# Kernel tuning notes

Measured on AMD Instinct MI355X. Metric: run time of the kernel, lower is better.

## Reference

```python
import jax, jax.numpy as jnp
import numpy as np

NEG_SLOPE = 0.2  # PyG GATConv default negative_slope


def gat_conv(x, src, dst, W, att_src, att_dst, bias, heads):
    """PyG-style GATConv (concat=True). src/dst already include self-loops.
    x: [N, Fin]; W: [Fin, heads*Fout]; att_*: [heads, Fout]; bias: [heads*Fout].
    """
    N = x.shape[0]
    Fout = att_src.shape[-1]
    h = (x @ W).reshape(N, heads, Fout)              # [N, H, C]
    a_s = jnp.einsum('nhc,hc->nh', h, att_src)        # [N, H]
    a_d = jnp.einsum('nhc,hc->nh', h, att_dst)        # [N, H]
    e = jax.nn.leaky_relu(a_s[src] + a_d[dst], NEG_SLOPE)   # [E, H]
    # segment softmax over destination nodes
    m = jax.lax.stop_gradient(jax.ops.segment_max(e, dst, num_segments=N))  # [N, H]
    ex = jnp.exp(e - m[dst])
    denom = jax.ops.segment_sum(ex, dst, num_segments=N)     # [N, H]
    alpha = ex / (denom[dst] + 1e-16)                          # [E, H]
    msg = h[src] * alpha[:, :, None]                           # [E, H, C]
    out = jax.ops.segment_sum(msg, dst, num_segments=N)       # [N, H, C]
    return out.reshape(N, heads * Fout) + bias


def setup_inputs() -> dict:
    key = jax.random.key(0)
    ks = jax.random.split(key, 16)
    NU, NS, D, H, CTX, B, E = 100000, 100000, 64, 2, 3, 512, 1600000
    inp = {
        'user_idx': jax.random.randint(ks[0], (B,), 0, NU),
        'context_idx': jax.random.randint(ks[1], (B, CTX), 0, NS),
        'edge_index': jax.random.randint(ks[2], (2, E), 0, NS),
        'user_emb': jax.random.normal(ks[3], (NU, D), jnp.float32),
        'service_emb': jax.random.normal(ks[4], (NS, D), jnp.float32),
        'W1': jax.random.normal(ks[5], (D, H * D), jnp.float32) / np.sqrt(D),
        'att_src1': jax.random.normal(ks[6], (H, D), jnp.float32) / np.sqrt(D),
        'att_dst1': jax.random.normal(ks[7], (H, D), jnp.float32) / np.sqrt(D),
        'b1': jnp.zeros((H * D,), jnp.float32),
        'W2': jax.random.normal(ks[8], (H * D, D), jnp.float32) / np.sqrt(H * D),
        'att_src2': jax.random.normal(ks[9], (1, D), jnp.float32) / np.sqrt(D),
        'att_dst2': jax.random.normal(ks[10], (1, D), jnp.float32) / np.sqrt(D),
        'b2': jnp.zeros((D,), jnp.float32),
        'fc_w': jax.random.normal(ks[11], (D * (CTX + 1), NS), jnp.float32) / np.sqrt(D * (CTX + 1)),
        'fc_b': jnp.zeros((NS,), jnp.float32),
    }
    return inp


def reference(user_idx, context_idx, edge_index, user_emb, service_emb,
              W1, att_src1, att_dst1, b1, W2, att_src2, att_dst2, b2, fc_w, fc_b):
    N = service_emb.shape[0]
    loops = jnp.arange(N)
    src = jnp.concatenate([edge_index[0], loops])  # add self loops (PyG default)
    dst = jnp.concatenate([edge_index[1], loops])
    user_vec = user_emb[user_idx]                                  # [B, D]
    g = gat_conv(service_emb, src, dst, W1, att_src1, att_dst1, b1, heads=2)
    g = jax.nn.elu(g)
    g = gat_conv(g, src, dst, W2, att_src2, att_dst2, b2, heads=1)  # [N, D]
    ctx = g[context_idx]                                            # [B, CTX, D]
    ctx = ctx.reshape(ctx.shape[0], -1)
    x = jnp.concatenate([user_vec, ctx], axis=1)                    # [B, D*(CTX+1)]
    return x @ fc_w + fc_b                                           # [B, num_services]
```

## Files before the change

kernel.cpp:

```cpp
#include <hip/hip_runtime.h>
#include <hip/hip_bf16.h>
#include <math.h>

#define NEG_SLOPE 0.2f

#define NPB 512
#define NPB_SH 9
#define SRC_BITS 18
#define LCAP 16384
#define BCAP 16384

typedef __attribute__((ext_vector_type(8))) short short8;
typedef __attribute__((ext_vector_type(4))) float f32x4;

__device__ __forceinline__ float leaky(float x) { return x > 0.f ? x : NEG_SLOPE * x; }

__device__ __forceinline__ unsigned short f2bf(float f) {
  unsigned u = __float_as_uint(f);
  unsigned r = (u + 0x7FFFu + ((u >> 16) & 1u)) >> 16;
  return (unsigned short)r;
}

#define LGKM_BARRIER()                                   \
  do {                                                   \
    asm volatile("s_waitcnt lgkmcnt(0)" ::: "memory");   \
    __builtin_amdgcn_s_barrier();                        \
  } while (0)

__global__ void k_h1(const float* __restrict__ x, const float* __restrict__ W1,
                     const float* __restrict__ att_src, const float* __restrict__ att_dst,
                     unsigned short* __restrict__ h1, float* __restrict__ a_s,
                     float* __restrict__ a_d, int N) {
  __shared__ __align__(16) float W1s[64 * 128];
  __shared__ __align__(16) float xs[32][64];
  const int tid = threadIdx.x;
  for (int i = tid; i < 64 * 128; i += 256) W1s[i] = W1[i];
  const int node0 = blockIdx.x * 32;
  for (int i = tid; i < 512; i += 256) {
    const int nn = node0 + (i >> 4);
    if (nn < N) ((float4*)xs)[i] = *(const float4*)(x + (size_t)nn * 64 + (i & 15) * 4);
  }
  const int ln  = tid >> 7;
  const int col = tid & 127;
  const int head = col >> 6;
  const int c = col & 63;
  const float as_w = att_src[head * 64 + c];
  const float ad_w = att_dst[head * 64 + c];
  __syncthreads();
  float wreg[64];
#pragma unroll
  for (int cc = 0; cc < 64; ++cc) wreg[cc] = W1s[cc * 128 + col];

  for (int it = 0; it < 16; ++it) {
    const int slot = it * 2 + ln;
    const int n = node0 + slot;
    if (n >= N) continue;
    float acc = 0.f;
#pragma unroll
    for (int q = 0; q < 16; ++q) {
      const float4 xv = *(const float4*)&xs[slot][q * 4];
      acc = fmaf(xv.x, wreg[q * 4 + 0], acc);
      acc = fmaf(xv.y, wreg[q * 4 + 1], acc);
      acc = fmaf(xv.z, wreg[q * 4 + 2], acc);
      acc = fmaf(xv.w, wreg[q * 4 + 3], acc);
    }
    h1[(size_t)n * 128 + col] = f2bf(acc);
    float vs = acc * as_w;
    float vd = acc * ad_w;
#pragma unroll
    for (int off = 32; off > 0; off >>= 1) {
      vs += __shfl_down(vs, off, 64);
      vd += __shfl_down(vd, off, 64);
    }
    if (c == 0) { a_s[n * 2 + head] = vs; a_d[n * 2 + head] = vd; }
  }
}

__global__ void k_init(int* __restrict__ cursor, int NB, int* __restrict__ flagC,
                       int* __restrict__ flag1, int* __restrict__ cnt, int N) {
  const int i = blockIdx.x * 256 + threadIdx.x;
  if (i < NB) cursor[i] = i * BCAP;
  if (i < N) { flagC[i] = 0; flag1[i] = 0; }
  if (i < 2) cnt[i] = 0;
}

__global__ void k_markC(const int* __restrict__ ctx, int nctx, int* __restrict__ flagC,
                        int* __restrict__ flag1) {
  const int i = blockIdx.x * 256 + threadIdx.x;
  if (i >= nctx) return;
  const int n = ctx[i];
  flagC[n] = 1;
  flag1[n] = 1;
}

__global__ void k_markS1e(const int* __restrict__ src, const int* __restrict__ dst,
                          int E, int Etot, const int* __restrict__ flagC,
                          int* __restrict__ flag1) {
  const int e = blockIdx.x * 256 + threadIdx.x;
  if (e >= Etot) return;
  int s, d;
  if (e < E) { s = src[e]; d = dst[e]; } else { s = d = e - E; }
  if (flagC[d]) flag1[s] = 1;
}

__global__ void k_compact(const int* __restrict__ flagC, const int* __restrict__ flag1,
                          int* __restrict__ listC, int* __restrict__ list1,
                          int* __restrict__ cnt, int N) {
  __shared__ int lc, l1, bc, b1;
  const int i = blockIdx.x * 256 + threadIdx.x;
  if (threadIdx.x == 0) { lc = 0; l1 = 0; }
  __syncthreads();
  int pc = -1, p1 = -1;
  if (i < N) {
    if (flagC[i]) pc = atomicAdd(&lc, 1);
    if (flag1[i]) p1 = atomicAdd(&l1, 1);
  }
  __syncthreads();
  if (threadIdx.x == 0) {
    bc = lc ? atomicAdd(&cnt[0], lc) : 0;
    b1 = l1 ? atomicAdd(&cnt[1], l1) : 0;
  }
  __syncthreads();
  if (pc >= 0) listC[bc + pc] = i;
  if (p1 >= 0) list1[b1 + p1] = i;
}

__global__ __launch_bounds__(1024) void k_bscatter(const int* __restrict__ src,
                                                   const int* __restrict__ dst, int E, int Etot,
                                                   int epb, const int* __restrict__ flag1,
                                                   int* __restrict__ cursor,
                                                   unsigned* __restrict__ rec, int NB) {
  __shared__ int hist[256];
  __shared__ int cur[256];
  const int tid = threadIdx.x;
  if (tid < 256) hist[tid] = 0;
  __syncthreads();
  const int e0 = blockIdx.x * epb;
  const int e1 = min(e0 + epb, Etot);
  for (int e = e0 + tid; e < e1; e += 1024) {
    const int d = (e < E) ? dst[e] : (e - E);
    if (flag1[d]) atomicAdd(&hist[d >> NPB_SH], 1);
  }
  __syncthreads();
  if (tid < NB) {
    const int c = hist[tid];
    cur[tid] = c ? atomicAdd(&cursor[tid], c) : 0;
  }
  __syncthreads();
  for (int e = e0 + tid; e < e1; e += 1024) {
    int sv, d;
    if (e < E) { sv = src[e]; d = dst[e]; } else { sv = d = e - E; }
    if (!flag1[d]) continue;
    const int b = d >> NPB_SH;
    const int p = atomicAdd(&cur[b], 1);
    rec[p] = (unsigned)sv | ((unsigned)(d & (NPB - 1)) << SRC_BITS);
  }
}

__global__ __launch_bounds__(1024) void k_bcsr(const unsigned* __restrict__ rec,
                                               const int* __restrict__ cursor,
                                               int* __restrict__ rowptr, int* __restrict__ adj,
                                               int N, int NB) {
  __shared__ int ldeg[NPB];
  __shared__ int s[NPB];
  __shared__ int ladj[LCAP];
  __shared__ int o0s, cnts;
  const int b = blockIdx.x;
  const int tid = threadIdx.x;

  if (tid < 256) s[tid] = (tid < NB) ? (cursor[tid] - tid * BCAP) : 0;
  __syncthreads();
  for (int off = 1; off < 256; off <<= 1) {
    int t = 0;
    if (tid < 256 && tid >= off) t = s[tid - off];
    __syncthreads();
    if (tid < 256) s[tid] += t;
    __syncthreads();
  }
  if (tid == 0) {
    const int cb = cursor[b] - b * BCAP;
    o0s = s[b] - cb;
    cnts = cb;
    if (b == 0) rowptr[N] = s[NB - 1];
  }
  __syncthreads();
  const int o0 = o0s;
  const int cnt = cnts;
  const int r0 = b * BCAP;

  if (tid < NPB) ldeg[tid] = 0;
  __syncthreads();
  for (int i = tid; i < cnt; i += 1024)
    atomicAdd(&ldeg[rec[r0 + i] >> SRC_BITS], 1);
  __syncthreads();
  int v = 0;
  if (tid < NPB) { v = ldeg[tid]; s[tid] = v; }
  __syncthreads();
  for (int off = 1; off < NPB; off <<= 1) {
    int t = 0;
    if (tid < NPB && tid >= off) t = s[tid - off];
    __syncthreads();
    if (tid < NPB) s[tid] += t;
    __syncthreads();
  }
  if (tid < NPB) {
    const int excl = s[tid] - v;
    const int node = b * NPB + tid;
    if (node < N) rowptr[node] = o0 + excl;
    ldeg[tid] = excl;
  }
  __syncthreads();
  if (cnt <= LCAP) {
    for (int i = tid; i < cnt; i += 1024) {
      const unsigned r = rec[r0 + i];
      const int p = atomicAdd(&ldeg[r >> SRC_BITS], 1);
      ladj[p] = (int)(r & ((1u << SRC_BITS) - 1));
    }
    __syncthreads();
    for (int i = tid; i < cnt; i += 1024) adj[o0 + i] = ladj[i];
  } else {
    for (int i = tid; i < cnt; i += 1024) {
      const unsigned r = rec[r0 + i];
      const int p = atomicAdd(&ldeg[r >> SRC_BITS], 1);
      adj[o0 + p] = (int)(r & ((1u << SRC_BITS) - 1));
    }
  }
}

__global__ void k_gat1(const unsigned short* __restrict__ h1, const float* __restrict__ as1,
                       const float* __restrict__ ad1, const int* __restrict__ rowptr,
                       const int* __restrict__ adj, const float* __restrict__ b1,
                       float* __restrict__ g, const int* __restrict__ list1,
                       const int* __restrict__ cnt) {
  const int w = threadIdx.x >> 6;
  const int l = threadIdx.x & 63;
  const int idx = blockIdx.x * 4 + w;
  if (idx >= cnt[1]) return;
  const int n = list1[idx];
  const int half = l >> 5;
  const int q = l & 31;
  const int head = q >> 4;
  const float adh = ad1[n * 2 + head];
  float a0 = 0.f, a1 = 0.f, a2 = 0.f, a3 = 0.f, dsum = 0.f;
  const int kb = rowptr[n], ke = rowptr[n + 1];
  const int kend = ke - 1;
  for (int k = kb + half; k < ke; k += 8) {
    const int e1 = k + 2, e2 = k + 4, e3 = k + 6;
    const int s0 = adj[k];
    const int s1 = adj[min(e1, kend)];
    const int s2 = adj[min(e2, kend)];
    const int s3 = adj[min(e3, kend)];
    const float x0 = as1[s0 * 2 + head] + adh;
    const float x1 = as1[s1 * 2 + head] + adh;
    const float x2 = as1[s2 * 2 + head] + adh;
    const float x3 = as1[s3 * 2 + head] + adh;
    const uint2 u0 = *(const uint2*)(h1 + (size_t)s0 * 128 + 4 * q);
    const uint2 u1 = *(const uint2*)(h1 + (size_t)s1 * 128 + 4 * q);
    const uint2 u2 = *(const uint2*)(h1 + (size_t)s2 * 128 + 4 * q);
    const uint2 u3 = *(const uint2*)(h1 + (size_t)s3 * 128 + 4 * q);
    const float w0 = __expf(leaky(x0));
    const float w1 = (e1 < ke) ? __expf(leaky(x1)) : 0.f;
    const float w2 = (e2 < ke) ? __expf(leaky(x2)) : 0.f;
    const float w3 = (e3 < ke) ? __expf(leaky(x3)) : 0.f;
    dsum += (w0 + w1) + (w2 + w3);
    a0 = fmaf(w0, __uint_as_float(u0.x << 16), a0);
    a1 = fmaf(w0, __uint_as_float(u0.x & 0xFFFF0000u), a1);
    a2 = fmaf(w0, __uint_as_float(u0.y << 16), a2);
    a3 = fmaf(w0, __uint_as_float(u0.y & 0xFFFF0000u), a3);
    a0 = fmaf(w1, __uint_as_float(u1.x << 16), a0);
    a1 = fmaf(w1, __uint_as_float(u1.x & 0xFFFF0000u), a1);
    a2 = fmaf(w1, __uint_as_float(u1.y << 16), a2);
    a3 = fmaf(w1, __uint_as_float(u1.y & 0xFFFF0000u), a3);
    a0 = fmaf(w2, __uint_as_float(u2.x << 16), a0);
    a1 = fmaf(w2, __uint_as_float(u2.x & 0xFFFF0000u), a1);
    a2 = fmaf(w2, __uint_as_float(u2.y << 16), a2);
    a3 = fmaf(w2, __uint_as_float(u2.y & 0xFFFF0000u), a3);
    a0 = fmaf(w3, __uint_as_float(u3.x << 16), a0);
    a1 = fmaf(w3, __uint_as_float(u3.x & 0xFFFF0000u), a1);
    a2 = fmaf(w3, __uint_as_float(u3.y << 16), a2);
    a3 = fmaf(w3, __uint_as_float(u3.y & 0xFFFF0000u), a3);
  }
  a0 += __shfl_xor(a0, 32, 64);
  a1 += __shfl_xor(a1, 32, 64);
  a2 += __shfl_xor(a2, 32, 64);
  a3 += __shfl_xor(a3, 32, 64);
  dsum += __shfl_xor(dsum, 32, 64);
  if (half == 0) {
    const float inv = 1.f / (dsum + 1e-16f);
    const float4 bv = *(const float4*)(b1 + 4 * q);
    float g0 = fmaf(a0, inv, bv.x);
    float g1 = fmaf(a1, inv, bv.y);
    float g2v = fmaf(a2, inv, bv.z);
    float g3 = fmaf(a3, inv, bv.w);
    g0 = g0 > 0.f ? g0 : expm1f(g0);
    g1 = g1 > 0.f ? g1 : expm1f(g1);
    g2v = g2v > 0.f ? g2v : expm1f(g2v);
    g3 = g3 > 0.f ? g3 : expm1f(g3);
    *(float4*)(g + (size_t)n * 128 + 4 * q) = make_float4(g0, g1, g2v, g3);
  }
}

__global__ void k_h2(const float* __restrict__ g, const float* __restrict__ W2,
                     const float* __restrict__ att_s, const float* __restrict__ att_d,
                     unsigned short* __restrict__ h2, float* __restrict__ a_s,
                     float* __restrict__ a_d, const int* __restrict__ list1,
                     const int* __restrict__ cnt) {
  const int cnt1 = cnt[1];
  const int base0 = blockIdx.x * 32;
  if (base0 >= cnt1) return;
  __shared__ __align__(16) float W2s[128 * 64];
  __shared__ __align__(16) float gs[2][128];
  __shared__ float part[2][64];
  for (int i = threadIdx.x; i < 128 * 64; i += 256) W2s[i] = W2[i];
  const int col = threadIdx.x & 63;
  const int kh  = (threadIdx.x >> 6) & 1;
  const int ln  = threadIdx.x >> 7;
  const float as_w = att_s[col], ad_w = att_d[col];
  __syncthreads();
  float wreg[64];
#pragma unroll
  for (int cc = 0; cc < 64; ++cc) wreg[cc] = W2s[(kh * 64 + cc) * 64 + col];

  for (int it = 0; it < 16; ++it) {
    const int sbase = base0 + it * 2;
    __syncthreads();
    {
      const int slot = sbase + (threadIdx.x >> 7);
      if (slot < cnt1) {
        const int nn = list1[slot];
        gs[threadIdx.x >> 7][threadIdx.x & 127] = g[(size_t)nn * 128 + (threadIdx.x & 127)];
      }
    }
    __syncthreads();
    const int slot = sbase + ln;
    const int n = (slot < cnt1) ? list1[slot] : -1;
    float acc = 0.f;
    if (n >= 0) {
#pragma unroll
      for (int q = 0; q < 16; ++q) {
        const float4 gv = *(const float4*)&gs[ln][kh * 64 + q * 4];
        acc = fmaf(gv.x, wreg[q * 4 + 0], acc);
        acc = fmaf(gv.y, wreg[q * 4 + 1], acc);
        acc = fmaf(gv.z, wreg[q * 4 + 2], acc);
        acc = fmaf(gv.w, wreg[q * 4 + 3], acc);
      }
    }
    if (kh == 1) part[ln][col] = acc;
    __syncthreads();
    if (kh == 0 && n >= 0) {
      acc += part[ln][col];
      h2[(size_t)n * 64 + col] = f2bf(acc);
      float vs = acc * as_w, vd = acc * ad_w;
#pragma unroll
      for (int off = 32; off > 0; off >>= 1) {
        vs += __shfl_down(vs, off, 64);
        vd += __shfl_down(vd, off, 64);
      }
      if (col == 0) { a_s[n] = vs; a_d[n] = vd; }
    }
  }
}

__global__ void k_gat2(const unsigned short* __restrict__ h2, const float* __restrict__ as2,
                       const float* __restrict__ ad2, const int* __restrict__ rowptr,
                       const int* __restrict__ adj, const float* __restrict__ b2,
                       float* __restrict__ g2, const int* __restrict__ listC,
                       const int* __restrict__ cnt) {
  const int w = threadIdx.x >> 6;
  const int l = threadIdx.x & 63;
  const int idx = blockIdx.x * 4 + w;
  if (idx >= cnt[0]) return;
  const int n = listC[idx];
  const int half = l >> 5;
  const int q = l & 31;
  const float adh = ad2[n];
  float a0 = 0.f, a1 = 0.f, dsum = 0.f;
  const int kb = rowptr[n], ke = rowptr[n + 1];
  const int kend = ke - 1;
  for (int k = kb + half; k < ke; k += 8) {
    const int e1 = k + 2, e2 = k + 4, e3 = k + 6;
    const int s0 = adj[k];
    const int s1 = adj[min(e1, kend)];
    const int s2 = adj[min(e2, kend)];
    const int s3 = adj[min(e3, kend)];
    const float x0 = as2[s0] + adh;
    const float x1 = as2[s1] + adh;
    const float x2 = as2[s2] + adh;
    const float x3 = as2[s3] + adh;
    const unsigned u0 = *(const unsigned*)(h2 + (size_t)s0 * 64 + 2 * q);
    const unsigned u1 = *(const unsigned*)(h2 + (size_t)s1 * 64 + 2 * q);
    const unsigned u2 = *(const unsigned*)(h2 + (size_t)s2 * 64 + 2 * q);
    const unsigned u3 = *(const unsigned*)(h2 + (size_t)s3 * 64 + 2 * q);
    const float w0 = __expf(leaky(x0));
    const float w1 = (e1 < ke) ? __expf(leaky(x1)) : 0.f;
    const float w2 = (e2 < ke) ? __expf(leaky(x2)) : 0.f;
    const float w3 = (e3 < ke) ? __expf(leaky(x3)) : 0.f;
    dsum += (w0 + w1) + (w2 + w3);
    a0 = fmaf(w0, __uint_as_float(u0 << 16), a0);
    a1 = fmaf(w0, __uint_as_float(u0 & 0xFFFF0000u), a1);
    a0 = fmaf(w1, __uint_as_float(u1 << 16), a0);
    a1 = fmaf(w1, __uint_as_float(u1 & 0xFFFF0000u), a1);
    a0 = fmaf(w2, __uint_as_float(u2 << 16), a0);
    a1 = fmaf(w2, __uint_as_float(u2 & 0xFFFF0000u), a1);
    a0 = fmaf(w3, __uint_as_float(u3 << 16), a0);
    a1 = fmaf(w3, __uint_as_float(u3 & 0xFFFF0000u), a1);
  }
  a0 += __shfl_xor(a0, 32, 64);
  a1 += __shfl_xor(a1, 32, 64);
  dsum += __shfl_xor(dsum, 32, 64);
  if (half == 0) {
    const float inv = 1.f / (dsum + 1e-16f);
    const float2 bv = *(const float2*)(b2 + 2 * q);
    ((float2*)g2)[(size_t)n * 32 + q] =
        make_float2(fmaf(a0, inv, bv.x), fmaf(a1, inv, bv.y));
  }
}

__global__ void k_xmat(const int* __restrict__ user_idx, const int* __restrict__ ctx_idx,
                       const float* __restrict__ user_emb, const float* __restrict__ g2,
                       unsigned short* __restrict__ xb) {
  const int b = blockIdx.x;
  const int k = threadIdx.x;
  float v;
  if (k < 64) {
    v = user_emb[(size_t)user_idx[b] * 64 + k];
  } else {
    const int c = (k - 64) >> 6;
    v = g2[(size_t)ctx_idx[b * 3 + c] * 64 + (k & 63)];
  }
  xb[(size_t)(k >> 5) * (512 * 32) + b * 32 + (k & 31)] = f2bf(v);
}

__global__ __launch_bounds__(1024) void k_fc(const unsigned short* __restrict__ xb,
                                             const float* __restrict__ fc_w,
                                             const float* __restrict__ fc_b,
                                             float* __restrict__ out, int NSRV,
                                             int ntiles, int gstride) {
  __shared__ __align__(16) unsigned short Blds[2][32 * 264];

  const int tid = threadIdx.x;
  const int w = tid >> 6;
  const int lane = tid & 63;
  const int l15 = lane & 15;
  const int kg = lane >> 4;

  if (blockIdx.x >= (unsigned)ntiles) return;

  short8 afr[2][8];
#pragma unroll
  for (int mf = 0; mf < 2; ++mf) {
    const int row = w * 32 + mf * 16 + l15;
#pragma unroll
    for (int ks = 0; ks < 8; ++ks) {
      afr[mf][ks] = *(const short8*)(xb + (size_t)ks * 16384 + row * 32 + kg * 8);
    }
  }

  const int sc  = tid & 31;
  const int sk0 = (tid >> 5) * 8;

  float v[8];
  auto loadv = [&](int t) {
    const int cg = t * 32 + sc;
    const bool okc = cg < NSRV;
#pragma unroll
    for (int i = 0; i < 8; ++i)
      v[i] = okc ? __builtin_nontemporal_load(fc_w + (size_t)(sk0 + i) * NSRV + cg) : 0.f;
  };
  auto writev = [&](int buf) {
    short8 lo;
#pragma unroll
    for (int i = 0; i < 8; ++i) lo[i] = (short)f2bf(v[i]);
    *(short8*)&Blds[buf][sc * 264 + sk0] = lo;
  };

  loadv(blockIdx.x);
  writev(0);
  if (blockIdx.x + gstride < ntiles) loadv(blockIdx.x + gstride);
  LGKM_BARRIER();

  int cur = 0;
  for (int t = blockIdx.x; t < ntiles; t += gstride) {
    if (t + gstride < ntiles) writev(cur ^ 1);
    if (t + 2 * gstride < ntiles) loadv(t + 2 * gstride);
    const int j0 = t * 32;
#pragma unroll
    for (int nf = 0; nf < 2; ++nf) {
      short8 bfr[8];
#pragma unroll
      for (int ks = 0; ks < 8; ++ks)
        bfr[ks] = *(const short8*)&Blds[cur][(nf * 16 + l15) * 264 + ks * 32 + kg * 8];
      f32x4 acc[2];
#pragma unroll
      for (int mf = 0; mf < 2; ++mf) acc[mf] = (f32x4){0.f, 0.f, 0.f, 0.f};
#pragma unroll
      for (int ks = 0; ks < 8; ++ks)
#pragma unroll
        for (int mf = 0; mf < 2; ++mf)
          acc[mf] = __builtin_amdgcn_mfma_f32_16x16x32_bf16(bfr[ks], afr[mf][ks], acc[mf], 0, 0, 0);
      const int jc = j0 + nf * 16 + kg * 4;
      if (j0 + 32 <= NSRV) {
        const float4 bias = *(const float4*)(fc_b + jc);
#pragma unroll
        for (int mf = 0; mf < 2; ++mf) {
          const int row = w * 32 + mf * 16 + l15;
          f32x4 o;
          o[0] = acc[mf][0] + bias.x;
          o[1] = acc[mf][1] + bias.y;
          o[2] = acc[mf][2] + bias.z;
          o[3] = acc[mf][3] + bias.w;
          __builtin_nontemporal_store(o, (f32x4*)(out + (size_t)row * NSRV + jc));
        }
      } else {
#pragma unroll
        for (int mf = 0; mf < 2; ++mf) {
          const int row = w * 32 + mf * 16 + l15;
#pragma unroll
          for (int r = 0; r < 4; ++r) {
            const int j = jc + r;
            if (j < NSRV) out[(size_t)row * NSRV + j] = acc[mf][r] + fc_b[j];
          }
        }
      }
    }
    LGKM_BARRIER();
    cur ^= 1;
  }
}

extern "C" void kernel_launch(void* const* d_in, const int* in_sizes, int n_in,
                              void* d_out, int out_size, void* d_ws, size_t ws_size,
                              hipStream_t stream) {
  const int* user_idx    = (const int*)d_in[0];
  const int* context_idx = (const int*)d_in[1];
  const int* edge_index  = (const int*)d_in[2];
  const float* user_emb  = (const float*)d_in[3];
  const float* service_emb = (const float*)d_in[4];
  const float* W1        = (const float*)d_in[5];
  const float* att_src1  = (const float*)d_in[6];
  const float* att_dst1  = (const float*)d_in[7];
  const float* b1        = (const float*)d_in[8];
  const float* W2        = (const float*)d_in[9];
  const float* att_src2  = (const float*)d_in[10];
  const float* att_dst2  = (const float*)d_in[11];
  const float* b2        = (const float*)d_in[12];
  const float* fc_w      = (const float*)d_in[13];
  const float* fc_b      = (const float*)d_in[14];
  float* out = (float*)d_out;

  const int B    = in_sizes[0];
  const int E    = in_sizes[2] / 2;
  const int N    = in_sizes[4] / 64;
  const int NSRV = in_sizes[14];
  const int Etot = E + N;
  const int NCTX = in_sizes[1];
  (void)B;

  const int* edge_src = edge_index;
  const int* edge_dst = edge_index + E;

  char* ws = (char*)d_ws;
  size_t off = 0;
  auto alloc = [&](size_t bytes) {
    void* p = ws + off;
    off = (off + bytes + 255) & ~(size_t)255;
    return p;
  };
  const int NB = (N + NPB - 1) >> NPB_SH;
  unsigned short* h1 = (unsigned short*)alloc((size_t)N * 128 * 2);
  float* g      = (float*)alloc((size_t)N * 128 * 4);
  float* as1    = (float*)alloc((size_t)N * 2 * 4);
  float* ad1    = (float*)alloc((size_t)N * 2 * 4);
  float* as2    = (float*)alloc((size_t)N * 4);
  float* ad2    = (float*)alloc((size_t)N * 4);
  int*   rowptr = (int*)alloc((size_t)(N + 1) * 4);
  int*   adj    = (int*)alloc((size_t)Etot * 4);
  unsigned* rec = (unsigned*)alloc((size_t)NB * BCAP * 4);
  int* bucketCursor = (int*)alloc(256 * 4);
  int* flagC  = (int*)alloc((size_t)N * 4);
  int* flag1  = (int*)alloc((size_t)N * 4);
  int* listC  = (int*)alloc((size_t)NCTX * 4);
  int* list1  = (int*)alloc((size_t)N * 4);
  int* cnt    = (int*)alloc(2 * 4);
  unsigned short* xb = (unsigned short*)alloc((size_t)512 * 256 * 2);
  unsigned short* h2 = h1;
  float* g2 = g;
  (void)ws_size;

  const int NBLK2 = 256;
  const int epb = (Etot + NBLK2 - 1) / NBLK2;
  const int nblk_N = (N + 255) / 256;
  const int nblk_E = (Etot + 255) / 256;

  k_init<<<nblk_N, 256, 0, stream>>>(bucketCursor, NB, flagC, flag1, cnt, N);

  k_h1<<<(N + 31) / 32, 256, 0, stream>>>(service_emb, W1, att_src1, att_dst1, h1, as1, ad1, N);

  k_markC<<<(NCTX + 255) / 256, 256, 0, stream>>>(context_idx, NCTX, flagC, flag1);
  k_markS1e<<<nblk_E, 256, 0, stream>>>(edge_src, edge_dst, E, Etot, flagC, flag1);
  k_compact<<<nblk_N, 256, 0, stream>>>(flagC, flag1, listC, list1, cnt, N);

  k_bscatter<<<NBLK2, 1024, 0, stream>>>(edge_src, edge_dst, E, Etot, epb, flag1, bucketCursor, rec, NB);
  k_bcsr<<<NB, 1024, 0, stream>>>(rec, bucketCursor, rowptr, adj, N, NB);

  k_gat1<<<(N + 3) / 4, 256, 0, stream>>>(h1, as1, ad1, rowptr, adj, b1, g, list1, cnt);

  k_h2<<<(N + 31) / 32, 256, 0, stream>>>(g, W2, att_src2, att_dst2, h2, as2, ad2, list1, cnt);

  k_gat2<<<(NCTX + 3) / 4, 256, 0, stream>>>(h2, as2, ad2, rowptr, adj, b2, g2, listC, cnt);

  k_xmat<<<512, 256, 0, stream>>>(user_idx, context_idx, user_emb, g2, xb);

  const int nfct = (NSRV + 31) / 32;
  const int grid = 512;
  k_fc<<<grid, 1024, 0, stream>>>(xb, fc_w, fc_b, out, NSRV, nfct, grid);
}
```

Measured before the change: 278.0 us.

## Fuse init and compaction into neighboring kernels; use persistent grids for gat1/h2

```diff
diff --git a/kernel.cpp b/kernel.cpp
--- a/kernel.cpp
+++ b/kernel.cpp
@@ -30,10 +30,17 @@
 __global__ void k_h1(const float* __restrict__ x, const float* __restrict__ W1,
                      const float* __restrict__ att_src, const float* __restrict__ att_dst,
                      unsigned short* __restrict__ h1, float* __restrict__ a_s,
-                     float* __restrict__ a_d, int N) {
+                     float* __restrict__ a_d, int N,
+                     int* __restrict__ cursor, int NB, int* __restrict__ flagC,
+                     int* __restrict__ flag1, int* __restrict__ cnt) {
+  const int tid = threadIdx.x;
+  const int gi = blockIdx.x * 256 + tid;
+  if (gi < N) { flagC[gi] = 0; flag1[gi] = 0; }
+  if (gi < NB) cursor[gi] = gi * BCAP;
+  if (gi < 2) cnt[gi] = 0;
+
   __shared__ __align__(16) float W1s[64 * 128];
   __shared__ __align__(16) float xs[32][64];
-  const int tid = threadIdx.x;
   for (int i = tid; i < 64 * 128; i += 256) W1s[i] = W1[i];
   const int node0 = blockIdx.x * 32;
   for (int i = tid; i < 512; i += 256) {
@@ -74,14 +81,6 @@
     }
     if (c == 0) { a_s[n * 2 + head] = vs; a_d[n * 2 + head] = vd; }
   }
-}
-
-__global__ void k_init(int* __restrict__ cursor, int NB, int* __restrict__ flagC,
-                       int* __restrict__ flag1, int* __restrict__ cnt, int N) {
-  const int i = blockIdx.x * 256 + threadIdx.x;
-  if (i < NB) cursor[i] = i * BCAP;
-  if (i < N) { flagC[i] = 0; flag1[i] = 0; }
-  if (i < 2) cnt[i] = 0;
 }
 
 __global__ void k_markC(const int* __restrict__ ctx, int nctx, int* __restrict__ flagC,
@@ -103,39 +102,40 @@
   if (flagC[d]) flag1[s] = 1;
 }
 
-__global__ void k_compact(const int* __restrict__ flagC, const int* __restrict__ flag1,
-                          int* __restrict__ listC, int* __restrict__ list1,
-                          int* __restrict__ cnt, int N) {
-  __shared__ int lc, l1, bc, b1;
-  const int i = blockIdx.x * 256 + threadIdx.x;
-  if (threadIdx.x == 0) { lc = 0; l1 = 0; }
-  __syncthreads();
-  int pc = -1, p1 = -1;
-  if (i < N) {
-    if (flagC[i]) pc = atomicAdd(&lc, 1);
-    if (flag1[i]) p1 = atomicAdd(&l1, 1);
-  }
-  __syncthreads();
-  if (threadIdx.x == 0) {
-    bc = lc ? atomicAdd(&cnt[0], lc) : 0;
-    b1 = l1 ? atomicAdd(&cnt[1], l1) : 0;
-  }
-  __syncthreads();
-  if (pc >= 0) listC[bc + pc] = i;
-  if (p1 >= 0) list1[b1 + p1] = i;
-}
-
-__global__ __launch_bounds__(1024) void k_bscatter(const int* __restrict__ src,
-                                                   const int* __restrict__ dst, int E, int Etot,
-                                                   int epb, const int* __restrict__ flag1,
-                                                   int* __restrict__ cursor,
-                                                   unsigned* __restrict__ rec, int NB) {
+__global__ __launch_bounds__(1024) void k_front(
+    const int* __restrict__ flagC, const int* __restrict__ flag1,
+    int* __restrict__ listC, int* __restrict__ list1, int* __restrict__ cnt,
+    int N, int nblkC,
+    const int* __restrict__ src, const int* __restrict__ dst, int E, int Etot,
+    int epb, int* __restrict__ cursor, unsigned* __restrict__ rec, int NB) {
   __shared__ int hist[256];
   __shared__ int cur[256];
   const int tid = threadIdx.x;
+
+  if ((int)blockIdx.x < nblkC) {
+    const int i = blockIdx.x * 1024 + tid;
+    if (tid == 0) { hist[0] = 0; hist[1] = 0; }
+    __syncthreads();
+    int pc = -1, p1 = -1;
+    if (i < N) {
+      if (flagC[i]) pc = atomicAdd(&hist[0], 1);
+      if (flag1[i]) p1 = atomicAdd(&hist[1], 1);
+    }
+    __syncthreads();
+    if (tid == 0) {
+      cur[0] = hist[0] ? atomicAdd(&cnt[0], hist[0]) : 0;
+      cur[1] = hist[1] ? atomicAdd(&cnt[1], hist[1]) : 0;
+    }
+    __syncthreads();
+    if (pc >= 0) listC[cur[0] + pc] = i;
+    if (p1 >= 0) list1[cur[1] + p1] = i;
+    return;
+  }
+
+  const int bb = blockIdx.x - nblkC;
   if (tid < 256) hist[tid] = 0;
   __syncthreads();
-  const int e0 = blockIdx.x * epb;
+  const int e0 = bb * epb;
   const int e1 = min(e0 + epb, Etot);
   for (int e = e0 + tid; e < e1; e += 1024) {
     const int d = (e < E) ? dst[e] : (e - E);
@@ -231,72 +231,73 @@
                        const float* __restrict__ ad1, const int* __restrict__ rowptr,
                        const int* __restrict__ adj, const float* __restrict__ b1,
                        float* __restrict__ g, const int* __restrict__ list1,
-                       const int* __restrict__ cnt) {
+                       const int* __restrict__ cnt, int gspan) {
   const int w = threadIdx.x >> 6;
   const int l = threadIdx.x & 63;
-  const int idx = blockIdx.x * 4 + w;
-  if (idx >= cnt[1]) return;
-  const int n = list1[idx];
   const int half = l >> 5;
   const int q = l & 31;
   const int head = q >> 4;
-  const float adh = ad1[n * 2 + head];
-  float a0 = 0.f, a1 = 0.f, a2 = 0.f, a3 = 0.f, dsum = 0.f;
-  const int kb = rowptr[n], ke = rowptr[n + 1];
-  const int kend = ke - 1;
-  for (int k = kb + half; k < ke; k += 8) {
-    const int e1 = k + 2, e2 = k + 4, e3 = k + 6;
-    const int s0 = adj[k];
-    const int s1 = adj[min(e1, kend)];
-    const int s2 = adj[min(e2, kend)];
-    const int s3 = adj[min(e3, kend)];
-    const float x0 = as1[s0 * 2 + head] + adh;
-    const float x1 = as1[s1 * 2 + head] + adh;
-    const float x2 = as1[s2 * 2 + head] + adh;
-    const float x3 = as1[s3 * 2 + head] + adh;
-    const uint2 u0 = *(const uint2*)(h1 + (size_t)s0 * 128 + 4 * q);
-    const uint2 u1 = *(const uint2*)(h1 + (size_t)s1 * 128 + 4 * q);
-    const uint2 u2 = *(const uint2*)(h1 + (size_t)s2 * 128 + 4 * q);
-    const uint2 u3 = *(const uint2*)(h1 + (size_t)s3 * 128 + 4 * q);
-    const float w0 = __expf(leaky(x0));
-    const float w1 = (e1 < ke) ? __expf(leaky(x1)) : 0.f;
-    const float w2 = (e2 < ke) ? __expf(leaky(x2)) : 0.f;
-    const float w3 = (e3 < ke) ? __expf(leaky(x3)) : 0.f;
-    dsum += (w0 + w1) + (w2 + w3);
-    a0 = fmaf(w0, __uint_as_float(u0.x << 16), a0);
-    a1 = fmaf(w0, __uint_as_float(u0.x & 0xFFFF0000u), a1);
-    a2 = fmaf(w0, __uint_as_float(u0.y << 16), a2);
-    a3 = fmaf(w0, __uint_as_float(u0.y & 0xFFFF0000u), a3);
-    a0 = fmaf(w1, __uint_as_float(u1.x << 16), a0);
-    a1 = fmaf(w1, __uint_as_float(u1.x & 0xFFFF0000u), a1);
-    a2 = fmaf(w1, __uint_as_float(u1.y << 16), a2);
-    a3 = fmaf(w1, __uint_as_float(u1.y & 0xFFFF0000u), a3);
-    a0 = fmaf(w2, __uint_as_float(u2.x << 16), a0);
-    a1 = fmaf(w2, __uint_as_float(u2.x & 0xFFFF0000u), a1);
-    a2 = fmaf(w2, __uint_as_float(u2.y << 16), a2);
-    a3 = fmaf(w2, __uint_as_float(u2.y & 0xFFFF0000u), a3);
-    a0 = fmaf(w3, __uint_as_float(u3.x << 16), a0);
-    a1 = fmaf(w3, __uint_as_float(u3.x & 0xFFFF0000u), a1);
-    a2 = fmaf(w3, __uint_as_float(u3.y << 16), a2);
-    a3 = fmaf(w3, __uint_as_float(u3.y & 0xFFFF0000u), a3);
-  }
-  a0 += __shfl_xor(a0, 32, 64);
-  a1 += __shfl_xor(a1, 32, 64);
-  a2 += __shfl_xor(a2, 32, 64);
-  a3 += __shfl_xor(a3, 32, 64);
-  dsum += __shfl_xor(dsum, 32, 64);
-  if (half == 0) {
-    const float inv = 1.f / (dsum + 1e-16f);
-    const float4 bv = *(const float4*)(b1 + 4 * q);
-    float g0 = fmaf(a0, inv, bv.x);
-    float g1 = fmaf(a1, inv, bv.y);
-    float g2v = fmaf(a2, inv, bv.z);
-    float g3 = fmaf(a3, inv, bv.w);
-    g0 = g0 > 0.f ? g0 : expm1f(g0);
-    g1 = g1 > 0.f ? g1 : expm1f(g1);
-    g2v = g2v > 0.f ? g2v : expm1f(g2v);
-    g3 = g3 > 0.f ? g3 : expm1f(g3);
-    *(float4*)(g + (size_t)n * 128 + 4 * q) = make_float4(g0, g1, g2v, g3);
+  const int cnt1 = cnt[1];
+  for (int idx = blockIdx.x * 4 + w; idx < cnt1; idx += gspan) {
+    const int n = list1[idx];
+    const float adh = ad1[n * 2 + head];
+    float a0 = 0.f, a1 = 0.f, a2 = 0.f, a3 = 0.f, dsum = 0.f;
+    const int kb = rowptr[n], ke = rowptr[n + 1];
+    const int kend = ke - 1;
+    for (int k = kb + half; k < ke; k += 8) {
+      const int e1 = k + 2, e2 = k + 4, e3 = k + 6;
+      const int s0 = adj[k];
+      const int s1 = adj[min(e1, kend)];
+      const int s2 = adj[min(e2, kend)];
+      const int s3 = adj[min(e3, kend)];
+      const float x0 = as1[s0 * 2 + head] + adh;
+      const float x1 = as1[s1 * 2 + head] + adh;
+      const float x2 = as1[s2 * 2 + head] + adh;
+      const float x3 = as1[s3 * 2 + head] + adh;
+      const uint2 u0 = *(const uint2*)(h1 + (size_t)s0 * 128 + 4 * q);
+      const uint2 u1 = *(const uint2*)(h1 + (size_t)s1 * 128 + 4 * q);
+      const uint2 u2 = *(const uint2*)(h1 + (size_t)s2 * 128 + 4 * q);
+      const uint2 u3 = *(const uint2*)(h1 + (size_t)s3 * 128 + 4 * q);
+      const float w0 = __expf(leaky(x0));
+      const float w1 = (e1 < ke) ? __expf(leaky(x1)) : 0.f;
+      const float w2 = (e2 < ke) ? __expf(leaky(x2)) : 0.f;
+      const float w3 = (e3 < ke) ? __expf(leaky(x3)) : 0.f;
+      dsum += (w0 + w1) + (w2 + w3);
+      a0 = fmaf(w0, __uint_as_float(u0.x << 16), a0);
+      a1 = fmaf(w0, __uint_as_float(u0.x & 0xFFFF0000u), a1);
+      a2 = fmaf(w0, __uint_as_float(u0.y << 16), a2);
+      a3 = fmaf(w0, __uint_as_float(u0.y & 0xFFFF0000u), a3);
+      a0 = fmaf(w1, __uint_as_float(u1.x << 16), a0);
+      a1 = fmaf(w1, __uint_as_float(u1.x & 0xFFFF0000u), a1);
+      a2 = fmaf(w1, __uint_as_float(u1.y << 16), a2);
+      a3 = fmaf(w1, __uint_as_float(u1.y & 0xFFFF0000u), a3);
+      a0 = fmaf(w2, __uint_as_float(u2.x << 16), a0);
+      a1 = fmaf(w2, __uint_as_float(u2.x & 0xFFFF0000u), a1);
+      a2 = fmaf(w2, __uint_as_float(u2.y << 16), a2);
+      a3 = fmaf(w2, __uint_as_float(u2.y & 0xFFFF0000u), a3);
+      a0 = fmaf(w3, __uint_as_float(u3.x << 16), a0);
+      a1 = fmaf(w3, __uint_as_float(u3.x & 0xFFFF0000u), a1);
+      a2 = fmaf(w3, __uint_as_float(u3.y << 16), a2);
+      a3 = fmaf(w3, __uint_as_float(u3.y & 0xFFFF0000u), a3);
+    }
+    a0 += __shfl_xor(a0, 32, 64);
+    a1 += __shfl_xor(a1, 32, 64);
+    a2 += __shfl_xor(a2, 32, 64);
+    a3 += __shfl_xor(a3, 32, 64);
+    dsum += __shfl_xor(dsum, 32, 64);
+    if (half == 0) {
+      const float inv = 1.f / (dsum + 1e-16f);
+      const float4 bv = *(const float4*)(b1 + 4 * q);
+      float g0 = fmaf(a0, inv, bv.x);
+      float g1 = fmaf(a1, inv, bv.y);
+      float g2v = fmaf(a2, inv, bv.z);
+      float g3 = fmaf(a3, inv, bv.w);
+      g0 = g0 > 0.f ? g0 : expm1f(g0);
+      g1 = g1 > 0.f ? g1 : expm1f(g1);
+      g2v = g2v > 0.f ? g2v : expm1f(g2v);
+      g3 = g3 > 0.f ? g3 : expm1f(g3);
+      *(float4*)(g + (size_t)n * 128 + 4 * q) = make_float4(g0, g1, g2v, g3);
+    }
   }
 }
 
@@ -306,8 +307,6 @@
                      float* __restrict__ a_d, const int* __restrict__ list1,
                      const int* __restrict__ cnt) {
   const int cnt1 = cnt[1];
-  const int base0 = blockIdx.x * 32;
-  if (base0 >= cnt1) return;
   __shared__ __align__(16) float W2s[128 * 64];
   __shared__ __align__(16) float gs[2][128];
   __shared__ float part[2][64];
@@ -321,42 +320,44 @@
 #pragma unroll
   for (int cc = 0; cc < 64; ++cc) wreg[cc] = W2s[(kh * 64 + cc) * 64 + col];
 
-  for (int it = 0; it < 16; ++it) {
-    const int sbase = base0 + it * 2;
-    __syncthreads();
-    {
-      const int slot = sbase + (threadIdx.x >> 7);
-      if (slot < cnt1) {
-        const int nn = list1[slot];
-        gs[threadIdx.x >> 7][threadIdx.x & 127] = g[(size_t)nn * 128 + (threadIdx.x & 127)];
+  for (int base0 = blockIdx.x * 32; base0 < cnt1; base0 += gridDim.x * 32) {
+    for (int it = 0; it < 16; ++it) {
+      const int sbase = base0 + it * 2;
+      __syncthreads();
+      {
+        const int slot = sbase + (threadIdx.x >> 7);
+        if (slot < cnt1) {
+          const int nn = list1[slot];
+          gs[threadIdx.x >> 7][threadIdx.x & 127] = g[(size_t)nn * 128 + (threadIdx.x & 127)];
+        }
       }
-    }
-    __syncthreads();
-    const int slot = sbase + ln;
-    const int n = (slot < cnt1) ? list1[slot] : -1;
-    float acc = 0.f;
-    if (n >= 0) {
-#pragma unroll
-      for (int q = 0; q < 16; ++q) {
-        const float4 gv = *(const float4*)&gs[ln][kh * 64 + q * 4];
-        acc = fmaf(gv.x, wreg[q * 4 + 0], acc);
-        acc = fmaf(gv.y, wreg[q * 4 + 1], acc);
-        acc = fmaf(gv.z, wreg[q * 4 + 2], acc);
-        acc = fmaf(gv.w, wreg[q * 4 + 3], acc);
+      __syncthreads();
+      const int slot = sbase + ln;
+      const int n = (slot < cnt1) ? list1[slot] : -1;
+      float acc = 0.f;
+      if (n >= 0) {
+#pragma unroll
+        for (int q = 0; q < 16; ++q) {
+          const float4 gv = *(const float4*)&gs[ln][kh * 64 + q * 4];
+          acc = fmaf(gv.x, wreg[q * 4 + 0], acc);
+          acc = fmaf(gv.y, wreg[q * 4 + 1], acc);
+          acc = fmaf(gv.z, wreg[q * 4 + 2], acc);
+          acc = fmaf(gv.w, wreg[q * 4 + 3], acc);
+        }
       }
-    }
-    if (kh == 1) part[ln][col] = acc;
-    __syncthreads();
-    if (kh == 0 && n >= 0) {
-      acc += part[ln][col];
-      h2[(size_t)n * 64 + col] = f2bf(acc);
-      float vs = acc * as_w, vd = acc * ad_w;
-#pragma unroll
-      for (int off = 32; off > 0; off >>= 1) {
-        vs += __shfl_down(vs, off, 64);
-        vd += __shfl_down(vd, off, 64);
+      if (kh == 1) part[ln][col] = acc;
+      __syncthreads();
+      if (kh == 0 && n >= 0) {
+        acc += part[ln][col];
+        h2[(size_t)n * 64 + col] = f2bf(acc);
+        float vs = acc * as_w, vd = acc * ad_w;
+#pragma unroll
+        for (int off = 32; off > 0; off >>= 1) {
+          vs += __shfl_down(vs, off, 64);
+          vd += __shfl_down(vd, off, 64);
+        }
+        if (col == 0) { a_s[n] = vs; a_d[n] = vd; }
       }
-      if (col == 0) { a_s[n] = vs; a_d[n] = vd; }
     }
   }
 }
@@ -589,23 +590,27 @@
 
   const int NBLK2 = 256;
   const int epb = (Etot + NBLK2 - 1) / NBLK2;
-  const int nblk_N = (N + 255) / 256;
   const int nblk_E = (Etot + 255) / 256;
-
-  k_init<<<nblk_N, 256, 0, stream>>>(bucketCursor, NB, flagC, flag1, cnt, N);
-
-  k_h1<<<(N + 31) / 32, 256, 0, stream>>>(service_emb, W1, att_src1, att_dst1, h1, as1, ad1, N);
+  const int nblkC = (N + 1023) / 1024;
+
+  k_h1<<<(N + 31) / 32, 256, 0, stream>>>(service_emb, W1, att_src1, att_dst1, h1, as1, ad1, N,
+                                          bucketCursor, NB, flagC, flag1, cnt);
 
   k_markC<<<(NCTX + 255) / 256, 256, 0, stream>>>(context_idx, NCTX, flagC, flag1);
   k_markS1e<<<nblk_E, 256, 0, stream>>>(edge_src, edge_dst, E, Etot, flagC, flag1);
-  k_compact<<<nblk_N, 256, 0, stream>>>(flagC, flag1, listC, list1, cnt, N);
-
-  k_bscatter<<<NBLK2, 1024, 0, stream>>>(edge_src, edge_dst, E, Etot, epb, flag1, bucketCursor, rec, NB);
+
+  k_front<<<nblkC + NBLK2, 1024, 0, stream>>>(flagC, flag1, listC, list1, cnt, N, nblkC,
+                                              edge_src, edge_dst, E, Etot, epb,
+                                              bucketCursor, rec, NB);
+
   k_bcsr<<<NB, 1024, 0, stream>>>(rec, bucketCursor, rowptr, adj, N, NB);
 
-  k_gat1<<<(N + 3) / 4, 256, 0, stream>>>(h1, as1, ad1, rowptr, adj, b1, g, list1, cnt);
-
-  k_h2<<<(N + 31) / 32, 256, 0, stream>>>(g, W2, att_src2, att_dst2, h2, as2, ad2, list1, cnt);
+  {
+    const int gb = 2048;
+    k_gat1<<<gb, 256, 0, stream>>>(h1, as1, ad1, rowptr, adj, b1, g, list1, cnt, gb * 4);
+  }
+
+  k_h2<<<1024, 256, 0, stream>>>(g, W2, att_src2, att_dst2, h2, as2, ad2, list1, cnt);
 
   k_gat2<<<(NCTX + 3) / 4, 256, 0, stream>>>(h2, as2, ad2, rowptr, adj, b2, g2, listC, cnt);
 
```

New measurement: 261.6 us. 5.9% less time.
